# Kernel optimization log

Measured on AMD Instinct MI355X. Metric: run time of the kernel, lower is better.

The kernel has to match this reference:

```python
import jax, jax.numpy as jnp
import numpy as np

KERNEL = 8
WEIGHT_INIT = np.array([0.49403, -0.44625, 0.82544, 0.99267, 1.6915, -2.0835, 2.9114,
                        -5.6555, 3.5984, -10.205, 20.828, -0.0022237, 0.0097854, 157.35],
                       dtype=np.float32)


def setup_inputs() -> dict:
    key = jax.random.key(0)
    x = jax.random.normal(key, (2048, 128, KERNEL, KERNEL), dtype=jnp.float32)
    weight = jnp.asarray(WEIGHT_INIT)
    return {"input": x, "weight": weight}


def reference(input, weight):
    eye = jnp.eye(KERNEL, dtype=input.dtype)  # serves as both mask and eye(8)
    # A = I - x @ x^T  over trailing two dims
    A = eye - jnp.matmul(input, jnp.swapaxes(input, 2, 3))
    B = jnp.matmul(A, A)
    C = jnp.matmul(B, A)
    D = jnp.matmul(C, A)
    E = jnp.matmul(D, A)
    F = jnp.matmul(E, A)
    G = jnp.matmul(F, A)
    Mat = (weight[0] * A + weight[1] * B + weight[2] * C + weight[3] * D
           + weight[4] * E + weight[5] * F + weight[6] * G + weight[7] * eye)
    return input + jnp.matmul(Mat, input)
```

## Files before the change

kernel.cpp:

```cpp
#include <hip/hip_runtime.h>


typedef float v2f __attribute__((ext_vector_type(2)));

__device__ __forceinline__ v2f pk_mul(v2f a, v2f b) {
    v2f d;
    asm("v_pk_mul_f32 %0, %1, %2" : "=v"(d) : "v"(a), "v"(b));
    return d;
}
__device__ __forceinline__ void pk_fma(v2f &acc, v2f a, v2f b) {
    asm("v_pk_fma_f32 %0, %1, %2, %0" : "+v"(acc) : "v"(a), "v"(b));
}
__device__ __forceinline__ v2f pk_mul_lo(v2f a, v2f b) {
    v2f d;
    asm("v_pk_mul_f32 %0, %1, %2 op_sel:[0,0] op_sel_hi:[0,1]"
        : "=v"(d) : "v"(a), "v"(b));
    return d;
}
__device__ __forceinline__ void pk_fma_lo(v2f &acc, v2f a, v2f b) {
    asm("v_pk_fma_f32 %0, %1, %2, %0 op_sel:[0,0,0] op_sel_hi:[0,1,1]"
        : "+v"(acc) : "v"(a), "v"(b));
}
__device__ __forceinline__ void pk_fma_hi(v2f &acc, v2f a, v2f b) {
    asm("v_pk_fma_f32 %0, %1, %2, %0 op_sel:[1,0,0] op_sel_hi:[1,1,1]"
        : "+v"(acc) : "v"(a), "v"(b));
}

__device__ __forceinline__ float pswap(float x)
{
    return __builtin_bit_cast(float,
        __builtin_amdgcn_update_dpp(0, __builtin_bit_cast(int, x),
                                    0xB1, 0xF, 0xF, true));
}

#define AE(p, q) A[(p) < (q) ? (p) : (q)][(p) < (q) ? (q) : (p)]

#define POW_STEP(wk)                                                      \
    {                                                                     \
        const v2f wv = (v2f){(wk), (wk)};                                 \
        _Pragma("unroll")                                                 \
        for (int j = 0; j < 2; ++j) {                                     \
            v2f n[8];                                                     \
            _Pragma("unroll")                                             \
            for (int p = 0; p < 8; ++p) {                                 \
                v2f a = pk_mul_lo(Ar[p][0], y[j][0]);                     \
                pk_fma_hi(a, Ar[p][0], y[j][1]);                          \
                pk_fma_lo(a, Ar[p][1], y[j][2]);                          \
                pk_fma_hi(a, Ar[p][1], y[j][3]);                          \
                pk_fma_lo(a, Ar[p][2], y[j][4]);                          \
                pk_fma_hi(a, Ar[p][2], y[j][5]);                          \
                pk_fma_lo(a, Ar[p][3], y[j][6]);                          \
                pk_fma_hi(a, Ar[p][3], y[j][7]);                          \
                n[p] = a;                                                 \
            }                                                             \
            _Pragma("unroll")                                             \
            for (int p = 0; p < 8; ++p) {                                 \
                y[j][p] = n[p];                                           \
                pk_fma(acc[j][p], wv, n[p]);                              \
            }                                                             \
        }                                                                 \
    }

__global__ __launch_bounds__(256)
void ns_poly_kernel(const float* __restrict__ in,
                    const float* __restrict__ wp,
                    float* __restrict__ out)
{
    __shared__ float4 lds[2048];

    const int tid  = threadIdx.x;
    const int wave = tid >> 6;
    const int lane = tid & 63;
    const int l    = lane >> 1;
    const int h    = lane & 1;

    const float w0 = wp[0], w1 = wp[1], w2 = wp[2], w3 = wp[3];
    const float w4 = wp[4], w5 = wp[5], w6 = wp[6], w7 = wp[7];

    const int wave_mat0 = blockIdx.x * 128 + wave * 32;
    const float4* __restrict__ gsrc =
        reinterpret_cast<const float4*>(in) + (size_t)wave_mat0 * 16;
    float4* __restrict__ gdst =
        reinterpret_cast<float4*>(out) + (size_t)wave_mat0 * 16;
    float4* L = lds + wave * 512;

#pragma unroll
    for (int it = 0; it < 8; ++it) {
        const int C  = it * 64 + lane;
        const int Cs = C ^ (((C >> 4) & 3) << 1);
        L[Cs] = gsrc[C];
    }
    asm volatile("s_waitcnt lgkmcnt(0)" ::: "memory");

    v2f y[2][8];
#pragma unroll
    for (int g = 0; g < 8; ++g) {
        const int f4 = (l * 16 + g * 2 + h) ^ ((l & 3) << 1);
        const float4 v = L[f4];
        y[0][g] = (v2f){v.x, v.y};
        y[1][g] = (v2f){v.z, v.w};
    }

    float S[8][8];
#pragma unroll
    for (int p = 0; p < 8; ++p)
#pragma unroll
        for (int q = p; q < 8; ++q) {
            v2f a = pk_mul(y[0][p], y[0][q]);
            pk_fma(a, y[1][p], y[1][q]);
            S[p][q] = a.x + a.y;
        }

    float A[8][8];
#pragma unroll
    for (int p = 0; p < 8; ++p)
#pragma unroll
        for (int q = p; q < 8; ++q) {
            const float other = pswap(S[p][q]);
            A[p][q] = (p == q ? 1.0f : 0.0f) - S[p][q] - other;
        }

    v2f Ar[8][4];
#pragma unroll
    for (int p = 0; p < 8; ++p)
#pragma unroll
        for (int jq = 0; jq < 4; ++jq)
            Ar[p][jq] = (v2f){AE(p, 2 * jq), AE(p, 2 * jq + 1)};

    v2f acc[2][8];
    const v2f w7v = (v2f){1.0f + w7, 1.0f + w7};
#pragma unroll
    for (int j = 0; j < 2; ++j)
#pragma unroll
        for (int p = 0; p < 8; ++p)
            acc[j][p] = pk_mul(w7v, y[j][p]);

    POW_STEP(w0);
    POW_STEP(w1);
    POW_STEP(w2);
    POW_STEP(w3);
    POW_STEP(w4);
    POW_STEP(w5);
    POW_STEP(w6);

#pragma unroll
    for (int g = 0; g < 8; ++g) {
        const int f4 = (l * 16 + g * 2 + h) ^ ((l & 3) << 1);
        L[f4] = make_float4(acc[0][g].x, acc[0][g].y,
                            acc[1][g].x, acc[1][g].y);
    }
    asm volatile("s_waitcnt lgkmcnt(0)" ::: "memory");

#pragma unroll
    for (int it = 0; it < 8; ++it) {
        const int C  = it * 64 + lane;
        const int Cs = C ^ (((C >> 4) & 3) << 1);
        gdst[C] = L[Cs];
    }
}

extern "C" void kernel_launch(void* const* d_in, const int* in_sizes, int n_in,
                              void* d_out, int out_size, void* d_ws, size_t ws_size,
                              hipStream_t stream)
{
    const float* in = (const float*)d_in[0];
    const float* w  = (const float*)d_in[1];
    float* outp     = (float*)d_out;

    const int nmat   = in_sizes[0] / 64;
    const int blocks = nmat / 128;
    ns_poly_kernel<<<blocks, 256, 0, stream>>>(in, w, outp);
}
```

Before: 119.6 us.

## Process four tiles per block with register prefetch of next tile

Each block now loops over four 128-matrix tiles instead of one, and prefetches the next tile's global data into registers while computing the current tile. The grid shrinks fourfold. This hides global load latency behind the polynomial compute and amortizes per-block setup. In exchange it raises register pressure through the prefetch buffer and leaves fewer blocks, 512 instead of 2048, to fill the GPU.

```diff
diff --git a/kernel.cpp b/kernel.cpp
--- a/kernel.cpp
+++ b/kernel.cpp
@@ -2,6 +2,8 @@
 
 
 typedef float v2f __attribute__((ext_vector_type(2)));
+
+#define NT 4
 
 __device__ __forceinline__ v2f pk_mul(v2f a, v2f b) {
     v2f d;
@@ -77,85 +79,102 @@
     const float w0 = wp[0], w1 = wp[1], w2 = wp[2], w3 = wp[3];
     const float w4 = wp[4], w5 = wp[5], w6 = wp[6], w7 = wp[7];
 
-    const int wave_mat0 = blockIdx.x * 128 + wave * 32;
-    const float4* __restrict__ gsrc =
-        reinterpret_cast<const float4*>(in) + (size_t)wave_mat0 * 16;
-    float4* __restrict__ gdst =
-        reinterpret_cast<float4*>(out) + (size_t)wave_mat0 * 16;
     float4* L = lds + wave * 512;
 
+    const size_t base0 =
+        ((size_t)blockIdx.x * NT * 128 + (size_t)wave * 32) * 16;
+    const float4* __restrict__ gin  = reinterpret_cast<const float4*>(in);
+    float4*       __restrict__ gout = reinterpret_cast<float4*>(out);
+
+    float4 r[8];
 #pragma unroll
-    for (int it = 0; it < 8; ++it) {
-        const int C  = it * 64 + lane;
-        const int Cs = C ^ (((C >> 4) & 3) << 1);
-        L[Cs] = gsrc[C];
-    }
-    asm volatile("s_waitcnt lgkmcnt(0)" ::: "memory");
+    for (int it = 0; it < 8; ++it)
+        r[it] = gin[base0 + it * 64 + lane];
 
-    v2f y[2][8];
+    for (int t = 0; t < NT; ++t) {
+        const size_t base = base0 + (size_t)t * 128 * 16;
+
+        asm volatile("s_waitcnt lgkmcnt(0)" ::: "memory");
+
 #pragma unroll
-    for (int g = 0; g < 8; ++g) {
-        const int f4 = (l * 16 + g * 2 + h) ^ ((l & 3) << 1);
-        const float4 v = L[f4];
-        y[0][g] = (v2f){v.x, v.y};
-        y[1][g] = (v2f){v.z, v.w};
-    }
-
-    float S[8][8];
-#pragma unroll
-    for (int p = 0; p < 8; ++p)
-#pragma unroll
-        for (int q = p; q < 8; ++q) {
-            v2f a = pk_mul(y[0][p], y[0][q]);
-            pk_fma(a, y[1][p], y[1][q]);
-            S[p][q] = a.x + a.y;
+        for (int it = 0; it < 8; ++it) {
+            const int C = it * 64 + lane;
+            L[C ^ (((C >> 4) & 3) << 1)] = r[it];
         }
 
-    float A[8][8];
+        if (t + 1 < NT) {
+            const size_t nbase = base + 128 * 16;
 #pragma unroll
-    for (int p = 0; p < 8; ++p)
-#pragma unroll
-        for (int q = p; q < 8; ++q) {
-            const float other = pswap(S[p][q]);
-            A[p][q] = (p == q ? 1.0f : 0.0f) - S[p][q] - other;
+            for (int it = 0; it < 8; ++it)
+                r[it] = gin[nbase + it * 64 + lane];
         }
 
-    v2f Ar[8][4];
+        asm volatile("s_waitcnt lgkmcnt(0)" ::: "memory");
+
+        v2f y[2][8];
 #pragma unroll
-    for (int p = 0; p < 8; ++p)
-#pragma unroll
-        for (int jq = 0; jq < 4; ++jq)
-            Ar[p][jq] = (v2f){AE(p, 2 * jq), AE(p, 2 * jq + 1)};
+        for (int g = 0; g < 8; ++g) {
+            const int f4 = (l * 16 + g * 2 + h) ^ ((l & 3) << 1);
+            const float4 v = L[f4];
+            y[0][g] = (v2f){v.x, v.y};
+            y[1][g] = (v2f){v.z, v.w};
+        }
 
-    v2f acc[2][8];
-    const v2f w7v = (v2f){1.0f + w7, 1.0f + w7};
-#pragma unroll
-    for (int j = 0; j < 2; ++j)
+        float S[8][8];
 #pragma unroll
         for (int p = 0; p < 8; ++p)
-            acc[j][p] = pk_mul(w7v, y[j][p]);
+#pragma unroll
+            for (int q = p; q < 8; ++q) {
+                v2f a = pk_mul(y[0][p], y[0][q]);
+                pk_fma(a, y[1][p], y[1][q]);
+                S[p][q] = a.x + a.y;
+            }
 
-    POW_STEP(w0);
-    POW_STEP(w1);
-    POW_STEP(w2);
-    POW_STEP(w3);
-    POW_STEP(w4);
-    POW_STEP(w5);
-    POW_STEP(w6);
+        float A[8][8];
+#pragma unroll
+        for (int p = 0; p < 8; ++p)
+#pragma unroll
+            for (int q = p; q < 8; ++q) {
+                const float other = pswap(S[p][q]);
+                A[p][q] = (p == q ? 1.0f : 0.0f) - S[p][q] - other;
+            }
+
+        v2f Ar[8][4];
+#pragma unroll
+        for (int p = 0; p < 8; ++p)
+#pragma unroll
+            for (int jq = 0; jq < 4; ++jq)
+                Ar[p][jq] = (v2f){AE(p, 2 * jq), AE(p, 2 * jq + 1)};
+
+        v2f acc[2][8];
+        const v2f w7v = (v2f){1.0f + w7, 1.0f + w7};
+#pragma unroll
+        for (int j = 0; j < 2; ++j)
+#pragma unroll
+            for (int p = 0; p < 8; ++p)
+                acc[j][p] = pk_mul(w7v, y[j][p]);
+
+        POW_STEP(w0);
+        POW_STEP(w1);
+        POW_STEP(w2);
+        POW_STEP(w3);
+        POW_STEP(w4);
+        POW_STEP(w5);
+        POW_STEP(w6);
 
 #pragma unroll
-    for (int g = 0; g < 8; ++g) {
-        const int f4 = (l * 16 + g * 2 + h) ^ ((l & 3) << 1);
-        L[f4] = make_float4(acc[0][g].x, acc[0][g].y,
-                            acc[1][g].x, acc[1][g].y);
-    }
-    asm volatile("s_waitcnt lgkmcnt(0)" ::: "memory");
+        for (int g = 0; g < 8; ++g) {
+            const int f4 = (l * 16 + g * 2 + h) ^ ((l & 3) << 1);
+            L[f4] = make_float4(acc[0][g].x, acc[0][g].y,
+                                acc[1][g].x, acc[1][g].y);
+        }
+        asm volatile("s_waitcnt lgkmcnt(0)" ::: "memory");
 
 #pragma unroll
-    for (int it = 0; it < 8; ++it) {
-        const int C  = it * 64 + lane;
-        const int Cs = C ^ (((C >> 4) & 3) << 1);
-        gdst[C] = L[Cs];
+        for (int it = 0; it < 8; ++it) {
+            const int C = it * 64 + lane;
+            gout[base + C] = L[C ^ (((C >> 4) & 3) << 1)];
+        }
     }
 }
 
@@ -168,6 +187,6 @@
     float* outp     = (float*)d_out;
 
     const int nmat   = in_sizes[0] / 64;
-    const int blocks = nmat / 128;
+    const int blocks = nmat / (128 * NT);
     ns_poly_kernel<<<blocks, 256, 0, stream>>>(in, w, outp);
 }
```

New measurement: 137.8 us. +15.2%, slower.
